# Performance work log

Measured on AMD Instinct MI355X. Metric: run time of the kernel, lower is better.

Reference implementation:

```python
import jax, jax.numpy as jnp
import numpy as np


def setup_inputs() -> dict:
    key = jax.random.key(0)
    ks = jax.random.split(key, 6)
    B, H, N, BS, W, T, D = 1, 32, 256, 32, 128, 4096, 128
    q = jax.random.normal(ks[0], (B, H, N * BS, D), dtype=jnp.float32)
    k_ctx = jax.random.normal(ks[1], (B, H, T, D), dtype=jnp.float32)
    v_ctx = jax.random.normal(ks[2], (B, H, T, D), dtype=jnp.float32)
    k_draft = jax.random.normal(ks[3], (B, H, N * BS, D), dtype=jnp.float32)
    v_draft = jax.random.normal(ks[4], (B, H, N * BS, D), dtype=jnp.float32)
    anchor_positions = jnp.sort(
        jax.random.randint(ks[5], (B, N), 0, T - BS), axis=-1
    )
    block_keep_mask = jnp.ones((B, N), dtype=bool)
    return {
        "q": q, "k_ctx": k_ctx, "v_ctx": v_ctx,
        "k_draft": k_draft, "v_draft": v_draft,
        "anchor_positions": anchor_positions,
        "block_keep_mask": block_keep_mask,
        "context_window": 128,
    }


def reference(q, k_ctx, v_ctx, k_draft, v_draft,
              anchor_positions, block_keep_mask, context_window):
    # FlashMTP block-sparse attention (FlexAttention mask_mod semantics):
    #   query block i attends to context tokens t in [max(0, a_i - W), a_i - 1]
    #   plus its own draft block (bidirectional); invalid blocks see nothing.
    B, H, Q, D = q.shape
    N = anchor_positions.shape[1]
    bs = Q // N
    T = k_ctx.shape[2]
    W = context_window
    scale = 1.0 / np.sqrt(D).astype(np.float32)

    # sliding context window indices per block: (B, N, W)
    idx = anchor_positions[:, :, None] - W + jnp.arange(W)[None, None, :]
    valid_ctx = idx >= 0  # idx < anchor always holds by construction
    idxc = jnp.clip(idx, 0, T - 1)
    gidx = idxc.reshape(B, 1, N * W, 1)
    k_win = jnp.take_along_axis(k_ctx, gidx, axis=2).reshape(B, H, N, W, D)
    v_win = jnp.take_along_axis(v_ctx, gidx, axis=2).reshape(B, H, N, W, D)

    qb = q.reshape(B, H, N, bs, D)
    kb = k_draft.reshape(B, H, N, bs, D)
    vb = v_draft.reshape(B, H, N, bs, D)

    s_ctx = jnp.einsum('bhnqd,bhnwd->bhnqw', qb, k_win) * scale
    s_blk = jnp.einsum('bhnqd,bhnkd->bhnqk', qb, kb) * scale

    keep = block_keep_mask[:, None, :, None, None]           # (B,1,N,1,1)
    m_ctx = valid_ctx[:, None, :, None, :] & keep            # (B,1,N,1,W)
    m_blk = jnp.broadcast_to(keep, (B, 1, N, 1, bs))         # (B,1,N,1,bs)
    mask = jnp.concatenate([m_ctx, m_blk], axis=-1)
    s = jnp.concatenate([s_ctx, s_blk], axis=-1)
    neg = jnp.asarray(-1e30, s.dtype)
    p = jax.nn.softmax(jnp.where(mask, s, neg), axis=-1)

    v_all = jnp.concatenate([v_win, vb], axis=3)             # (B,H,N,W+bs,D)
    out = jnp.einsum('bhnqk,bhnkd->bhnqd', p, v_all)
    out = out * keep.astype(out.dtype)  # invalid blocks -> zero output
    return out.reshape(B, H, Q, D)
```

## Files before the change

kernel.cpp:

```cpp
#include <hip/hip_runtime.h>

constexpr int H_  = 32;
constexpr int N_  = 256;
constexpr int BS_ = 32;
constexpr int W_  = 128;
constexpr int T_  = 4096;
constexpr int D_  = 128;
constexpr int NQ_ = 8192;
constexpr float SCALE_  = 0.08838834764831845f;
constexpr float L2E_    = 1.4426950408889634f;
constexpr float MFLOOR_ = -1.0e28f;
constexpr float DEFER_  = 8.0f;

typedef __attribute__((ext_vector_type(4))) float f4;
typedef __attribute__((ext_vector_type(4))) short s4;
typedef __attribute__((ext_vector_type(8))) short s8;
typedef __attribute__((ext_vector_type(4))) float fx4;
typedef __attribute__((ext_vector_type(2))) int i2;

__device__ __forceinline__ int pack2(float a, float b) {
  int r;
  asm("v_cvt_pk_bf16_f32 %0, %1, %2" : "=v"(r) : "v"(a), "v"(b));
  return r;
}

union frag_u { int w[4]; s8 v; };

__device__ __forceinline__ void lds_barrier() {
  asm volatile("s_waitcnt lgkmcnt(0)" ::: "memory");
  __builtin_amdgcn_s_barrier();
}

__global__ __launch_bounds__(128, 2)
void mtp_attn_kernel(const float* __restrict__ q,
                     const float* __restrict__ k_ctx,
                     const float* __restrict__ v_ctx,
                     const float* __restrict__ k_draft,
                     const float* __restrict__ v_draft,
                     const int* __restrict__ anchor,
                     const int* __restrict__ keepm,
                     float* __restrict__ out)
{
  int u = blockIdx.x;
  u = (u & 7) * 1024 + (u >> 3);
  const int h = u >> 8;
  const int n = u & 255;

  const int tu   = threadIdx.x;
  const int lane = tu & 63;
  const int wu   = tu >> 6;
  const int l15  = lane & 15;
  const int g    = lane >> 4;
  const int rb   = tu >> 5;
  const int c4   = tu & 31;

  const int A  = anchor[n];
  const int kp = keepm[n];
  const int wm = W_ - A;

  __shared__ __align__(16) unsigned char smem_[17664];
  short* kb = (short*)smem_;
  short* vT = (short*)(smem_ + 8448);

  const float* qrow = q + ((size_t)h * NQ_ + (size_t)n * BS_ + wu * 16 + l15) * D_;
  s8 qb[4];
#pragma unroll
  for (int ks = 0; ks < 4; ++ks) {
    f4 f0 = *reinterpret_cast<const f4*>(qrow + ks * 32 + g * 4);
    f4 f1 = *reinterpret_cast<const f4*>(qrow + ks * 32 + 16 + g * 4);
    frag_u uq;
    uq.w[0] = pack2(f0[0], f0[1]); uq.w[1] = pack2(f0[2], f0[3]);
    uq.w[2] = pack2(f1[0], f1[1]); uq.w[3] = pack2(f1[2], f1[3]);
    qb[ks] = uq.v;
  }

  const float* kcb = k_ctx + (size_t)h * T_ * D_;
  const float* vcb = v_ctx + (size_t)h * T_ * D_;
  const float* kdb = k_draft + ((size_t)h * NQ_ + (size_t)n * BS_) * D_;
  const float* vdb = v_draft + ((size_t)h * NQ_ + (size_t)n * BS_) * D_;

  auto loadK = [&](f4 (&dst)[8], int c) {
#pragma unroll
    for (int i = 0; i < 8; ++i) {
      int row = i * 4 + rb;
      const float* src;
      if (c < 4) { int idx = A - W_ + c * 32 + row; idx = idx < 0 ? 0 : idx; src = kcb + (size_t)idx * D_; }
      else       { src = kdb + (size_t)row * D_; }
      dst[i] = reinterpret_cast<const f4*>(src)[c4];
    }
  };
  auto loadV = [&](f4 (&dst)[8], int c) {
#pragma unroll
    for (int p = 0; p < 2; ++p)
#pragma unroll
      for (int i = 0; i < 4; ++i) {
        int row = p * 16 + rb * 4 + i;
        const float* src;
        if (c < 4) { int idx = A - W_ + c * 32 + row; idx = idx < 0 ? 0 : idx; src = vcb + (size_t)idx * D_; }
        else       { src = vdb + (size_t)row * D_; }
        dst[p * 4 + i] = reinterpret_cast<const f4*>(src)[c4];
      }
  };

  f4 krA[8], vrA[8], krB[8], vrB[8];
  loadK(krA, 0); loadV(vrA, 0);
  loadK(krB, 1); loadV(vrB, 1);

  float m  = -3.0e38f;
  float ls = 0.0f;
  fx4 oacc[8];
#pragma unroll
  for (int t = 0; t < 8; ++t) oacc[t] = {0.f, 0.f, 0.f, 0.f};

#pragma unroll
  for (int c = 0; c < 5; ++c) {
    f4 (&kr)[8] = (c & 1) ? krB : krA;
    f4 (&vr)[8] = (c & 1) ? vrB : vrA;

    lds_barrier();
#pragma unroll
    for (int i = 0; i < 8; ++i) {
      i2 w = { pack2(kr[i][0], kr[i][1]), pack2(kr[i][2], kr[i][3]) };
      *reinterpret_cast<i2*>(kb + (i * 4 + rb) * 132 + c4 * 4) = w;
    }
#pragma unroll
    for (int p = 0; p < 2; ++p) {
      int keyl = p * 16 + rb * 4;
#pragma unroll
      for (int j = 0; j < 4; ++j) {
        i2 w = { pack2(vr[p * 4 + 0][j], vr[p * 4 + 1][j]),
                 pack2(vr[p * 4 + 2][j], vr[p * 4 + 3][j]) };
        *reinterpret_cast<i2*>(vT + (c4 * 4 + j) * 36 + keyl) = w;
      }
    }
    if (c < 3) { loadK(kr, c + 2); loadV(vr, c + 2); }
    lds_barrier();

    fx4 st[2] = { {0.f,0.f,0.f,0.f}, {0.f,0.f,0.f,0.f} };
    __builtin_amdgcn_s_setprio(1);
#pragma unroll
    for (int ks = 0; ks < 4; ++ks) {
#pragma unroll
      for (int t2 = 0; t2 < 2; ++t2) {
        const short* kpr = kb + (t2 * 16 + l15) * 132 + ks * 32 + g * 4;
        s4 b0 = *reinterpret_cast<const s4*>(kpr);
        s4 b1 = *reinterpret_cast<const s4*>(kpr + 16);
        s8 kf = { b0[0], b0[1], b0[2], b0[3], b1[0], b1[1], b1[2], b1[3] };
        st[t2] = __builtin_amdgcn_mfma_f32_16x16x32_bf16(kf, qb[ks], st[t2], 0, 0, 0);
      }
    }
    __builtin_amdgcn_s_setprio(0);

    float sv[2][4];
    float cm = -3.0e38f;
#pragma unroll
    for (int t2 = 0; t2 < 2; ++t2) {
      int kb0 = c * 32 + t2 * 16 + g * 4;
#pragma unroll
      for (int r = 0; r < 4; ++r) {
        float v = st[t2][r] * SCALE_;
        bool valid = (c == 4) || (kb0 + r >= wm);
        v = valid ? v : -1.0e30f;
        sv[t2][r] = v;
        cm = fmaxf(cm, v);
      }
    }
    cm = fmaxf(cm, __shfl_xor(cm, 16));
    cm = fmaxf(cm, __shfl_xor(cm, 32));

    if (c == 0) {
      m = fmaxf(cm, MFLOOR_);
    } else {
      float pm = fmaxf(m, cm);
      if (!__all(pm - m <= DEFER_)) {
        float mn = fmaxf(pm, MFLOOR_);
        float al = exp2f((m - mn) * L2E_);
        ls *= al;
        float alr[4];
#pragma unroll
        for (int r = 0; r < 4; ++r) alr[r] = __shfl(al, g * 4 + r);
#pragma unroll
        for (int nt = 0; nt < 8; ++nt)
#pragma unroll
          for (int r = 0; r < 4; ++r) oacc[nt][r] *= alr[r];
        m = mn;
      }
    }

    float pv[8];
#pragma unroll
    for (int t2 = 0; t2 < 2; ++t2)
#pragma unroll
      for (int r = 0; r < 4; ++r) {
        float p = exp2f((sv[t2][r] - m) * L2E_);
        ls += p;
        pv[t2 * 4 + r] = p;
      }
    frag_u up;
    up.w[0] = pack2(pv[0], pv[1]); up.w[1] = pack2(pv[2], pv[3]);
    up.w[2] = pack2(pv[4], pv[5]); up.w[3] = pack2(pv[6], pv[7]);
    s8 pa = up.v;

    __builtin_amdgcn_s_setprio(1);
#pragma unroll
    for (int nt = 0; nt < 8; ++nt) {
      const short* vp = vT + (nt * 16 + l15) * 36 + g * 4;
      s4 b0 = *reinterpret_cast<const s4*>(vp);
      s4 b1 = *reinterpret_cast<const s4*>(vp + 16);
      s8 vb2 = { b0[0], b0[1], b0[2], b0[3], b1[0], b1[1], b1[2], b1[3] };
      oacc[nt] = __builtin_amdgcn_mfma_f32_16x16x32_bf16(pa, vb2, oacc[nt], 0, 0, 0);
    }
    __builtin_amdgcn_s_setprio(0);
  }

  ls += __shfl_xor(ls, 16);
  ls += __shfl_xor(ls, 32);
  float linv[4];
#pragma unroll
  for (int r = 0; r < 4; ++r) {
    float lq = __shfl(ls, g * 4 + r);
    linv[r] = kp ? (1.0f / lq) : 0.0f;
  }
  float* ob = out + ((size_t)h * NQ_ + (size_t)n * BS_ + wu * 16 + g * 4) * D_ + l15;
#pragma unroll
  for (int nt = 0; nt < 8; ++nt)
#pragma unroll
    for (int r = 0; r < 4; ++r)
      ob[(size_t)r * D_ + nt * 16] = oacc[nt][r] * linv[r];
}

extern "C" void kernel_launch(void* const* d_in, const int* in_sizes, int n_in,
                              void* d_out, int out_size, void* d_ws, size_t ws_size,
                              hipStream_t stream) {
  (void)in_sizes; (void)n_in; (void)d_ws; (void)ws_size; (void)out_size;
  const float* q       = (const float*)d_in[0];
  const float* k_ctx   = (const float*)d_in[1];
  const float* v_ctx   = (const float*)d_in[2];
  const float* k_draft = (const float*)d_in[3];
  const float* v_draft = (const float*)d_in[4];
  const int*   anchor  = (const int*)d_in[5];
  const int*   keep    = (const int*)d_in[6];
  float*       out     = (float*)d_out;
  mtp_attn_kernel<<<dim3(8192), dim3(128), 0, stream>>>(
      q, k_ctx, v_ctx, k_draft, v_draft, anchor, keep, out);
}
```

Baseline: 158.2 us.

## Load K fragments straight to registers and double-buffer V in LDS

Measured after the change: 219.7 us. +38.8%, slower.

```diff
diff --git a/kernel.cpp b/kernel.cpp
--- a/kernel.cpp
+++ b/kernel.cpp
@@ -58,9 +58,9 @@
   const int kp = keepm[n];
   const int wm = W_ - A;
 
-  __shared__ __align__(16) unsigned char smem_[17664];
-  short* kb = (short*)smem_;
-  short* vT = (short*)(smem_ + 8448);
+  __shared__ __align__(16) unsigned char smem_[18432];
+  short* vT0 = (short*)smem_;
+  short* vT1 = (short*)(smem_ + 9216);
 
   const float* qrow = q + ((size_t)h * NQ_ + (size_t)n * BS_ + wu * 16 + l15) * D_;
   s8 qb[4];
@@ -79,17 +79,10 @@
   const float* kdb = k_draft + ((size_t)h * NQ_ + (size_t)n * BS_) * D_;
   const float* vdb = v_draft + ((size_t)h * NQ_ + (size_t)n * BS_) * D_;
 
-  auto loadK = [&](f4 (&dst)[8], int c) {
-#pragma unroll
-    for (int i = 0; i < 8; ++i) {
-      int row = i * 4 + rb;
-      const float* src;
-      if (c < 4) { int idx = A - W_ + c * 32 + row; idx = idx < 0 ? 0 : idx; src = kcb + (size_t)idx * D_; }
-      else       { src = kdb + (size_t)row * D_; }
-      dst[i] = reinterpret_cast<const f4*>(src)[c4];
-    }
-  };
-  auto loadV = [&](f4 (&dst)[8], int c) {
+  f4 vr[8];
+  f4 kf[16];
+
+  auto loadV = [&](int c) {
 #pragma unroll
     for (int p = 0; p < 2; ++p)
 #pragma unroll
@@ -98,13 +91,43 @@
         const float* src;
         if (c < 4) { int idx = A - W_ + c * 32 + row; idx = idx < 0 ? 0 : idx; src = vcb + (size_t)idx * D_; }
         else       { src = vdb + (size_t)row * D_; }
-        dst[p * 4 + i] = reinterpret_cast<const f4*>(src)[c4];
+        vr[p * 4 + i] = reinterpret_cast<const f4*>(src)[c4];
       }
   };
-
-  f4 krA[8], vrA[8], krB[8], vrB[8];
-  loadK(krA, 0); loadV(vrA, 0);
-  loadK(krB, 1); loadV(vrB, 1);
+  auto loadK = [&](int c) {
+    const float* s0; const float* s1;
+    if (c < 4) {
+      int i0 = A - W_ + c * 32 + l15;  int i1 = i0 + 16;
+      i0 = i0 < 0 ? 0 : i0;            i1 = i1 < 0 ? 0 : i1;
+      s0 = kcb + (size_t)i0 * D_;      s1 = kcb + (size_t)i1 * D_;
+    } else {
+      s0 = kdb + (size_t)l15 * D_;     s1 = s0 + 16 * D_;
+    }
+#pragma unroll
+    for (int ks = 0; ks < 4; ++ks) {
+      kf[ks * 2 + 0]     = reinterpret_cast<const f4*>(s0)[ks * 8 + g];
+      kf[ks * 2 + 1]     = reinterpret_cast<const f4*>(s0)[ks * 8 + 4 + g];
+      kf[8 + ks * 2 + 0] = reinterpret_cast<const f4*>(s1)[ks * 8 + g];
+      kf[8 + ks * 2 + 1] = reinterpret_cast<const f4*>(s1)[ks * 8 + 4 + g];
+    }
+  };
+  auto writeV = [&](short* buf) {
+#pragma unroll
+    for (int p = 0; p < 2; ++p) {
+      int keyl = p * 16 + rb * 4;
+#pragma unroll
+      for (int j = 0; j < 4; ++j) {
+        i2 w = { pack2(vr[p * 4 + 0][j], vr[p * 4 + 1][j]),
+                 pack2(vr[p * 4 + 2][j], vr[p * 4 + 3][j]) };
+        *reinterpret_cast<i2*>(buf + (c4 * 4 + j) * 36 + keyl) = w;
+      }
+    }
+  };
+
+  loadV(0);
+  loadK(0);
+  writeV(vT0);
+  loadV(1);
 
   float m  = -3.0e38f;
   float ls = 0.0f;
@@ -112,44 +135,28 @@
 #pragma unroll
   for (int t = 0; t < 8; ++t) oacc[t] = {0.f, 0.f, 0.f, 0.f};
 
+  lds_barrier();
+
 #pragma unroll
   for (int c = 0; c < 5; ++c) {
-    f4 (&kr)[8] = (c & 1) ? krB : krA;
-    f4 (&vr)[8] = (c & 1) ? vrB : vrA;
-
-    lds_barrier();
-#pragma unroll
-    for (int i = 0; i < 8; ++i) {
-      i2 w = { pack2(kr[i][0], kr[i][1]), pack2(kr[i][2], kr[i][3]) };
-      *reinterpret_cast<i2*>(kb + (i * 4 + rb) * 132 + c4 * 4) = w;
-    }
-#pragma unroll
-    for (int p = 0; p < 2; ++p) {
-      int keyl = p * 16 + rb * 4;
-#pragma unroll
-      for (int j = 0; j < 4; ++j) {
-        i2 w = { pack2(vr[p * 4 + 0][j], vr[p * 4 + 1][j]),
-                 pack2(vr[p * 4 + 2][j], vr[p * 4 + 3][j]) };
-        *reinterpret_cast<i2*>(vT + (c4 * 4 + j) * 36 + keyl) = w;
-      }
-    }
-    if (c < 3) { loadK(kr, c + 2); loadV(vr, c + 2); }
-    lds_barrier();
+    if (c < 4) writeV((c & 1) ? vT0 : vT1);
+    if (c < 3) loadV(c + 2);
 
     fx4 st[2] = { {0.f,0.f,0.f,0.f}, {0.f,0.f,0.f,0.f} };
     __builtin_amdgcn_s_setprio(1);
 #pragma unroll
-    for (int ks = 0; ks < 4; ++ks) {
-#pragma unroll
-      for (int t2 = 0; t2 < 2; ++t2) {
-        const short* kpr = kb + (t2 * 16 + l15) * 132 + ks * 32 + g * 4;
-        s4 b0 = *reinterpret_cast<const s4*>(kpr);
-        s4 b1 = *reinterpret_cast<const s4*>(kpr + 16);
-        s8 kf = { b0[0], b0[1], b0[2], b0[3], b1[0], b1[1], b1[2], b1[3] };
-        st[t2] = __builtin_amdgcn_mfma_f32_16x16x32_bf16(kf, qb[ks], st[t2], 0, 0, 0);
-      }
-    }
+    for (int t2 = 0; t2 < 2; ++t2)
+#pragma unroll
+      for (int ks = 0; ks < 4; ++ks) {
+        f4 f0 = kf[t2 * 8 + ks * 2 + 0];
+        f4 f1 = kf[t2 * 8 + ks * 2 + 1];
+        frag_u uk;
+        uk.w[0] = pack2(f0[0], f0[1]); uk.w[1] = pack2(f0[2], f0[3]);
+        uk.w[2] = pack2(f1[0], f1[1]); uk.w[3] = pack2(f1[2], f1[3]);
+        st[t2] = __builtin_amdgcn_mfma_f32_16x16x32_bf16(uk.v, qb[ks], st[t2], 0, 0, 0);
+      }
     __builtin_amdgcn_s_setprio(0);
+    if (c < 4) loadK(c + 1);
 
     float sv[2][4];
     float cm = -3.0e38f;
@@ -201,16 +208,19 @@
     up.w[2] = pack2(pv[4], pv[5]); up.w[3] = pack2(pv[6], pv[7]);
     s8 pa = up.v;
 
+    const short* vb = (c & 1) ? vT1 : vT0;
     __builtin_amdgcn_s_setprio(1);
 #pragma unroll
     for (int nt = 0; nt < 8; ++nt) {
-      const short* vp = vT + (nt * 16 + l15) * 36 + g * 4;
+      const short* vp = vb + (nt * 16 + l15) * 36 + g * 4;
       s4 b0 = *reinterpret_cast<const s4*>(vp);
       s4 b1 = *reinterpret_cast<const s4*>(vp + 16);
       s8 vb2 = { b0[0], b0[1], b0[2], b0[3], b1[0], b1[1], b1[2], b1[3] };
       oacc[nt] = __builtin_amdgcn_mfma_f32_16x16x32_bf16(pa, vb2, oacc[nt], 0, 0, 0);
     }
     __builtin_amdgcn_s_setprio(0);
+
+    if (c < 4) lds_barrier();
   }
 
   ls += __shfl_xor(ls, 16);
```

## Double-buffer K/V tiles in LDS and drop one barrier per chunk

Applied to the files above, without the earlier changes.

Result: faster. 152.6 us (-3.5%).

```diff
diff --git a/kernel.cpp b/kernel.cpp
--- a/kernel.cpp
+++ b/kernel.cpp
@@ -58,9 +58,9 @@
   const int kp = keepm[n];
   const int wm = W_ - A;
 
-  __shared__ __align__(16) unsigned char smem_[17664];
-  short* kb = (short*)smem_;
-  short* vT = (short*)(smem_ + 8448);
+  __shared__ __align__(16) unsigned char smem_[35328];
+  short* Kb[2] = { (short*)smem_,          (short*)(smem_ + 8448) };
+  short* Vb[2] = { (short*)(smem_ + 16896), (short*)(smem_ + 16896 + 9216) };
 
   const float* qrow = q + ((size_t)h * NQ_ + (size_t)n * BS_ + wu * 16 + l15) * D_;
   s8 qb[4];
@@ -79,14 +79,22 @@
   const float* kdb = k_draft + ((size_t)h * NQ_ + (size_t)n * BS_) * D_;
   const float* vdb = v_draft + ((size_t)h * NQ_ + (size_t)n * BS_) * D_;
 
+  f4 krA[8], vrA[8], krB[8], vrB[8];
+
   auto loadK = [&](f4 (&dst)[8], int c) {
-#pragma unroll
-    for (int i = 0; i < 8; ++i) {
-      int row = i * 4 + rb;
-      const float* src;
-      if (c < 4) { int idx = A - W_ + c * 32 + row; idx = idx < 0 ? 0 : idx; src = kcb + (size_t)idx * D_; }
-      else       { src = kdb + (size_t)row * D_; }
-      dst[i] = reinterpret_cast<const f4*>(src)[c4];
+    if (c < 4) {
+      int base = (A - W_ + c * 32) * 32;
+      const f4* kc4 = reinterpret_cast<const f4*>(kcb);
+#pragma unroll
+      for (int i = 0; i < 8; ++i) {
+        int off = base + tu + 128 * i;
+        off = off < 0 ? 0 : off;
+        dst[i] = kc4[off];
+      }
+    } else {
+      const f4* kd4 = reinterpret_cast<const f4*>(kdb);
+#pragma unroll
+      for (int i = 0; i < 8; ++i) dst[i] = kd4[tu + 128 * i];
     }
   };
   auto loadV = [&](f4 (&dst)[8], int c) {
@@ -101,10 +109,31 @@
         dst[p * 4 + i] = reinterpret_cast<const f4*>(src)[c4];
       }
   };
-
-  f4 krA[8], vrA[8], krB[8], vrB[8];
+  auto writeK = [&](f4 (&src)[8], short* kb) {
+#pragma unroll
+    for (int i = 0; i < 8; ++i) {
+      int row = (tu >> 5) + 4 * i;
+      i2 w = { pack2(src[i][0], src[i][1]), pack2(src[i][2], src[i][3]) };
+      *reinterpret_cast<i2*>(kb + row * 132 + c4 * 4) = w;
+    }
+  };
+  auto writeV = [&](f4 (&src)[8], short* vT) {
+#pragma unroll
+    for (int p = 0; p < 2; ++p) {
+      int keyl = p * 16 + rb * 4;
+#pragma unroll
+      for (int j = 0; j < 4; ++j) {
+        i2 w = { pack2(src[p * 4 + 0][j], src[p * 4 + 1][j]),
+                 pack2(src[p * 4 + 2][j], src[p * 4 + 3][j]) };
+        *reinterpret_cast<i2*>(vT + (c4 * 4 + j) * 36 + keyl) = w;
+      }
+    }
+  };
+
   loadK(krA, 0); loadV(vrA, 0);
   loadK(krB, 1); loadV(vrB, 1);
+  writeK(krA, Kb[0]); writeV(vrA, Vb[0]);
+  loadK(krA, 2); loadV(vrA, 2);
 
   float m  = -3.0e38f;
   float ls = 0.0f;
@@ -112,30 +141,19 @@
 #pragma unroll
   for (int t = 0; t < 8; ++t) oacc[t] = {0.f, 0.f, 0.f, 0.f};
 
+  lds_barrier();
+
 #pragma unroll
   for (int c = 0; c < 5; ++c) {
-    f4 (&kr)[8] = (c & 1) ? krB : krA;
-    f4 (&vr)[8] = (c & 1) ? vrB : vrA;
-
-    lds_barrier();
-#pragma unroll
-    for (int i = 0; i < 8; ++i) {
-      i2 w = { pack2(kr[i][0], kr[i][1]), pack2(kr[i][2], kr[i][3]) };
-      *reinterpret_cast<i2*>(kb + (i * 4 + rb) * 132 + c4 * 4) = w;
-    }
-#pragma unroll
-    for (int p = 0; p < 2; ++p) {
-      int keyl = p * 16 + rb * 4;
-#pragma unroll
-      for (int j = 0; j < 4; ++j) {
-        i2 w = { pack2(vr[p * 4 + 0][j], vr[p * 4 + 1][j]),
-                 pack2(vr[p * 4 + 2][j], vr[p * 4 + 3][j]) };
-        *reinterpret_cast<i2*>(vT + (c4 * 4 + j) * 36 + keyl) = w;
-      }
-    }
-    if (c < 3) { loadK(kr, c + 2); loadV(vr, c + 2); }
-    lds_barrier();
-
+    if (c < 4) {
+      f4 (&kw)[8] = ((c + 1) & 1) ? krB : krA;
+      f4 (&vw)[8] = ((c + 1) & 1) ? vrB : vrA;
+      writeK(kw, Kb[(c + 1) & 1]);
+      writeV(vw, Vb[(c + 1) & 1]);
+      if (c < 3) { loadK(kw, c + 3); loadV(vw, c + 3); }
+    }
+
+    const short* kb = Kb[c & 1];
     fx4 st[2] = { {0.f,0.f,0.f,0.f}, {0.f,0.f,0.f,0.f} };
     __builtin_amdgcn_s_setprio(1);
 #pragma unroll
@@ -201,6 +219,7 @@
     up.w[2] = pack2(pv[4], pv[5]); up.w[3] = pack2(pv[6], pv[7]);
     s8 pa = up.v;
 
+    const short* vT = Vb[c & 1];
     __builtin_amdgcn_s_setprio(1);
 #pragma unroll
     for (int nt = 0; nt < 8; ++nt) {
@@ -211,6 +230,8 @@
       oacc[nt] = __builtin_amdgcn_mfma_f32_16x16x32_bf16(pa, vb2, oacc[nt], 0, 0, 0);
     }
     __builtin_amdgcn_s_setprio(0);
+
+    if (c < 4) lds_barrier();
   }
 
   ls += __shfl_xor(ls, 16);
```
